# Kernel tuning notes

Measured on AMD Instinct MI355X. Metric: run time of the kernel, lower is better.

Reference implementation:

```python
import jax, jax.numpy as jnp
import numpy as np

N = 10000   # num nodes
E = 160000  # num edges (avg degree 16)
B = 8       # batch dim carried on node state
D = 64      # hidden_size


def setup_inputs() -> dict:
    key = jax.random.key(0)
    k1, k2, k3, k4, k5, k6 = jax.random.split(key, 6)
    state = jax.random.normal(k1, (N, B, D), jnp.float32)
    feature = jax.random.normal(k2, (N, 32), jnp.float32)  # unused by GAT math, kept for call signature
    weight = jax.random.normal(k3, (2 * D, D), jnp.float32) * 0.05
    src = jax.random.randint(k4, (E,), 0, N, jnp.int32)
    dst = jax.random.randint(k5, (E,), 0, N, jnp.int32)
    dist = jax.random.uniform(k6, (E, 1), jnp.float32)
    return dict(state=state, feature=feature, weight=weight, src=src, dst=dst, dist=dist)


def reference(state, feature, weight, src, dst, dist):
    # --- msg_edge: gather src/dst node states per edge ---
    src_state = state[src]                 # [E,B,D]
    dst_state = state[dst]                 # [E,B,D]
    es = jnp.concatenate([src_state, dst_state], axis=-1)          # [E,B,2D]
    alpha = jax.nn.leaky_relu(jnp.einsum('ebk,kd->ebd', es, weight),
                              negative_slope=0.2)                  # tf.nn.leaky_relu alpha=0.2
    alpha = alpha * dist[:, :, None]       # dist [E,1] broadcast to [E,1,1]

    # --- msg_reduce: segment softmax over incoming edges of each dst node ---
    amax = jax.ops.segment_max(alpha, dst, num_segments=N)         # [N,B,D]
    ex = jnp.exp(alpha - amax[dst])                                # stable exp
    denom = jax.ops.segment_sum(ex, dst, num_segments=N)           # [N,B,D]
    attn = ex / denom[dst]                                         # [E,B,D]

    # weighted sum of src states scattered back to dst nodes, then relu
    new_state = jax.nn.relu(jax.ops.segment_sum(attn * src_state, dst, num_segments=N))
    return new_state
```

## Files before the change

kernel.cpp:

```cpp
#include <hip/hip_runtime.h>
#include <hip/hip_fp16.h>
#include <math.h>

#define N_NODES 10000
#define N_EDGES 160000
#define B_ 8
#define D_ 64
#define BD 512
#define CAP 48
#define CAPR 56

typedef _Float16 f16x8 __attribute__((ext_vector_type(8)));
typedef float f32x4 __attribute__((ext_vector_type(4)));
typedef float f4v __attribute__((ext_vector_type(4)));
typedef unsigned int u32;

union HU { _Float16 f; unsigned short u; };
union HC { u32 u; __half2 h; };

__global__ void __launch_bounds__(256, 4) prep_kernel(
    const int* __restrict__ src, const int* __restrict__ dst,
    const float* __restrict__ dist, int* __restrict__ counts, u32* __restrict__ bucket,
    const float* __restrict__ state, const float* __restrict__ weight,
    u32* __restrict__ G, __half* __restrict__ Pd) {
    __shared__ _Float16 At[64 * 72];
    __shared__ char smemB[128 * 72 * 2];
    _Float16* Bt = (_Float16*)smemB;
    unsigned short* Ps2 = (unsigned short*)smemB;
    unsigned short* Ps  = (unsigned short*)(smemB + 8704);
    int bid = blockIdx.x;
    int tid = threadIdx.x;

    int s_e, d_e; float di_e;
    bool do_edge = tid < 128;
    if (do_edge) {
        int e = bid * 128 + tid;
        s_e = src[e];
        d_e = dst[e];
        di_e = dist[e];
    }

    int row0 = bid * 64;
    int wave = tid >> 6, lane = tid & 63;
    int quad = lane >> 4, m16 = lane & 15;
    int m_loc = wave * 16 + m16;

    const f4v* st4 = (const f4v*)(state + (size_t)row0 * 64);
    for (int i = tid; i < 1024; i += 256) {
        int r = i >> 4, c4 = (i & 15) << 2;
        f4v v = __builtin_nontemporal_load(&st4[i]);
        union { short4 s; _Float16 h[4]; } u;
        u.h[0] = (_Float16)v[0]; u.h[1] = (_Float16)v[1];
        u.h[2] = (_Float16)v[2]; u.h[3] = (_Float16)v[3];
        *(short4*)&At[r * 72 + c4] = u.s;
    }
    const f4v* w4 = (const f4v*)weight;
    for (int i = tid; i < 2048; i += 256) {
        int r = i >> 4, c4 = (i & 15) << 2;
        f4v v = w4[i];
        int h = r >> 6, k = r & 63;
        int nb = h * 64 + c4;
        Bt[(nb + 0) * 72 + k] = (_Float16)v[0];
        Bt[(nb + 1) * 72 + k] = (_Float16)v[1];
        Bt[(nb + 2) * 72 + k] = (_Float16)v[2];
        Bt[(nb + 3) * 72 + k] = (_Float16)v[3];
    }

    if (do_edge) {
        int pos = atomicAdd(&counts[d_e], 1);
        if (pos < CAP) {
            unsigned short hd = __half_as_ushort(__float2half_rn(di_e * 1.44269504f));
            bucket[d_e * CAPR + pos] = (u32)s_e | ((u32)hd << 16);
        }
    }
    __syncthreads();

    f16x8 bf0[8], bf1[8];
#pragma unroll
    for (int tcol = 0; tcol < 8; tcol++) {
        int n = tcol * 16 + m16;
        bf0[tcol] = *(const f16x8*)&Bt[n * 72 + quad * 8];
        bf1[tcol] = *(const f16x8*)&Bt[n * 72 + 32 + quad * 8];
    }
    f16x8 a0 = *(const f16x8*)&At[m_loc * 72 + quad * 8];
    f16x8 a1 = *(const f16x8*)&At[m_loc * 72 + 32 + quad * 8];
    __syncthreads();

#pragma unroll
    for (int tcol = 0; tcol < 8; tcol++) {
        int n = tcol * 16 + m16;
        f32x4 acc = {0.f, 0.f, 0.f, 0.f};
        acc = __builtin_amdgcn_mfma_f32_16x16x32_f16(a0, bf0[tcol], acc, 0, 0, 0);
        acc = __builtin_amdgcn_mfma_f32_16x16x32_f16(a1, bf1[tcol], acc, 0, 0, 0);
#pragma unroll
        for (int r = 0; r < 4; r++) {
            int ml = wave * 16 + quad * 4 + r;
            unsigned short ph = __half_as_ushort(__float2half_rn(acc[r]));
            if (tcol < 4) Ps2[ml * 68 + n] = ph;
            else          Ps[ml * 64 + (n - 64)] = ph;
        }
    }
    __syncthreads();

    const u32* Ps2w = (const u32*)Ps2;
    const u32* Atw = (const u32*)At;
    for (int i = tid; i < 1024; i += 256) {
        int row = i >> 4, q = i & 15;
        int m = row0 + row;
        size_t base = (size_t)(m >> 3) * 512 + (size_t)(m & 7) * 64;
        u32 p01 = Ps2w[row * 34 + q * 2];
        u32 p23 = Ps2w[row * 34 + q * 2 + 1];
        u32 x01 = Atw[row * 36 + q * 2];
        u32 x23 = Atw[row * 36 + q * 2 + 1];
        float4 v = make_float4(__uint_as_float(p01), __uint_as_float(p23),
                               __uint_as_float(x01), __uint_as_float(x23));
        *(float4*)&G[base + q * 4] = v;
    }
    for (int i = tid; i < 512; i += 256) {
        int row = i >> 3, seg = i & 7;
        int m = row0 + row;
        size_t base = (size_t)(m >> 3) * 512 + (size_t)(m & 7) * 64;
        *(float4*)&Pd[base + seg * 8] = *(const float4*)&Ps[row * 64 + seg * 8];
    }
}

__global__ void __launch_bounds__(256) gat_aggregate(
    const u32* __restrict__ G,
    const __half* __restrict__ Pds,
    const int* __restrict__ counts,
    const u32* __restrict__ bucket,
    float* __restrict__ out) {
    int wave = threadIdx.x >> 6;
    int lane = threadIdx.x & 63;
    int n = (blockIdx.x << 2) + wave;

    int offA = lane * 4;
    int offB = offA + 256;

    int cnt = counts[n]; if (cnt > CAP) cnt = CAP;
    const u32* ep = bucket + n * CAPR;

    union { double d; __half2 h[2]; } pdA, pdB;
    pdA.d = *(const double*)(Pds + (size_t)n * 512 + offA);
    pdB.d = *(const double*)(Pds + (size_t)n * 512 + offB);

    const __half2 c06 = __float2half2_rn(0.6f);
    const __half2 c04 = __float2half2_rn(0.4f);
    __half2 zero = __float2half2_rn(0.f);
    __half2 lA0 = zero, lA1 = zero, oA0 = zero, oA1 = zero;
    __half2 lB0 = zero, lB1 = zero, oB0 = zero, oB1 = zero;

    auto lrexp = [&](__half2 z, __half2 dd) -> __half2 {
        HC zz, az; zz.h = z;
        az.u = zz.u & 0x7fff7fffu;
        __half2 lk = __hfma2(az.h, c04, __hmul2(z, c06));
        __half2 aa = __hmul2(lk, dd);
        return __halves2half2(hexp2(__low2half(aa)), hexp2(__high2half(aa)));
    };

    auto body = [&](float4 g1, float4 g2, __half2 dd) {
        union { float4 f; __half2 h[4]; } u1, u2; u1.f = g1; u2.f = g2;
        __half2 e;
        e = lrexp(__hadd2(u1.h[0], pdA.h[0]), dd); lA0 = __hadd2(lA0, e); oA0 = __hfma2(e, u1.h[2], oA0);
        e = lrexp(__hadd2(u1.h[1], pdA.h[1]), dd); lA1 = __hadd2(lA1, e); oA1 = __hfma2(e, u1.h[3], oA1);
        e = lrexp(__hadd2(u2.h[0], pdB.h[0]), dd); lB0 = __hadd2(lB0, e); oB0 = __hfma2(e, u2.h[2], oB0);
        e = lrexp(__hadd2(u2.h[1], pdB.h[1]), dd); lB1 = __hadd2(lB1, e); oB1 = __hfma2(e, u2.h[3], oB1);
    };

    for (int j = 0; j < cnt; j += 2) {
        u32 ra = ep[j];
        bool two = (j + 1) < cnt;
        u32 rb = two ? ep[j + 1] : 0u;
        const u32* pa = G + (size_t)(ra & 0xffffu) * 512;
        float4 ga1 = *(const float4*)(pa + offA);
        float4 ga2 = *(const float4*)(pa + offB);
        float4 gb1, gb2;
        if (two) {
            const u32* pb = G + (size_t)(rb & 0xffffu) * 512;
            gb1 = *(const float4*)(pb + offA);
            gb2 = *(const float4*)(pb + offB);
        }
        __half ha = __ushort_as_half((unsigned short)(ra >> 16));
        body(ga1, ga2, __halves2half2(ha, ha));
        if (two) {
            __half hb = __ushort_as_half((unsigned short)(rb >> 16));
            body(gb1, gb2, __halves2half2(hb, hb));
        }
    }

    float* op = out + (size_t)n * BD;
    float4 rA, rB;
    if (cnt > 0) {
        rA.x = fmaxf(__low2float(oA0)  * __builtin_amdgcn_rcpf(__low2float(lA0)),  0.f);
        rA.y = fmaxf(__high2float(oA0) * __builtin_amdgcn_rcpf(__high2float(lA0)), 0.f);
        rA.z = fmaxf(__low2float(oA1)  * __builtin_amdgcn_rcpf(__low2float(lA1)),  0.f);
        rA.w = fmaxf(__high2float(oA1) * __builtin_amdgcn_rcpf(__high2float(lA1)), 0.f);
        rB.x = fmaxf(__low2float(oB0)  * __builtin_amdgcn_rcpf(__low2float(lB0)),  0.f);
        rB.y = fmaxf(__high2float(oB0) * __builtin_amdgcn_rcpf(__high2float(lB0)), 0.f);
        rB.z = fmaxf(__low2float(oB1)  * __builtin_amdgcn_rcpf(__low2float(lB1)),  0.f);
        rB.w = fmaxf(__high2float(oB1) * __builtin_amdgcn_rcpf(__high2float(lB1)), 0.f);
    } else {
        rA = make_float4(0.f, 0.f, 0.f, 0.f);
        rB = rA;
    }
    *(float4*)(op + offA) = rA;
    *(float4*)(op + offB) = rB;
}

extern "C" void kernel_launch(void* const* d_in, const int* in_sizes, int n_in,
                              void* d_out, int out_size, void* d_ws, size_t ws_size,
                              hipStream_t stream) {
    const float* state  = (const float*)d_in[0];
    const float* weight = (const float*)d_in[2];
    const int*   src    = (const int*)d_in[3];
    const int*   dst    = (const int*)d_in[4];
    const float* dist   = (const float*)d_in[5];

    u32*    G      = (u32*)d_ws;
    __half* Pd     = (__half*)(G + (size_t)N_NODES * 512);
    u32*    bucket = (u32*)(Pd + (size_t)N_NODES * 512);
    int*    counts = (int*)(bucket + (size_t)N_NODES * CAPR);

    hipMemsetAsync(bucket, 0, ((size_t)N_NODES * CAPR + N_NODES) * sizeof(u32), stream);
    prep_kernel<<<1250, 256, 0, stream>>>(src, dst, dist, counts, bucket,
                                          state, weight, G, Pd);
    gat_aggregate<<<2500, 256, 0, stream>>>(G, Pd, counts, bucket, (float*)d_out);
}
```

Measured before the change: 146.2 us.

## Split gather table into four batch-pair planes and process two edges per wave

The gathered node table G and the Pd buffer are reorganised into four planes, each holding two of the eight batch slices per node. Each aggregate block now handles one plane, and the two halves of a wave process alternate edges, combined at the end with a cross-lane shuffle. The intent is a smaller per-plane working set that fits better in cache during random gathers, and more blocks for parallelism. The cost is four times as many blocks, repeated bucket and count reads per plane, and an odd-count padding trick that reads node 0's row and subtracts its contribution.

```diff
diff --git a/kernel.cpp b/kernel.cpp
--- a/kernel.cpp
+++ b/kernel.cpp
@@ -107,7 +107,9 @@
     for (int i = tid; i < 1024; i += 256) {
         int row = i >> 4, q = i & 15;
         int m = row0 + row;
-        size_t base = (size_t)(m >> 3) * 512 + (size_t)(m & 7) * 64;
+        int b = m & 7;
+        size_t base = (size_t)(b >> 1) * (N_NODES * 128)
+                    + (size_t)(m >> 3) * 128 + (size_t)(b & 1) * 64;
         u32 p01 = Ps2w[row * 34 + q * 2];
         u32 p23 = Ps2w[row * 34 + q * 2 + 1];
         u32 x01 = Atw[row * 36 + q * 2];
@@ -119,7 +121,9 @@
     for (int i = tid; i < 512; i += 256) {
         int row = i >> 3, seg = i & 7;
         int m = row0 + row;
-        size_t base = (size_t)(m >> 3) * 512 + (size_t)(m & 7) * 64;
+        int b = m & 7;
+        size_t base = (size_t)(b >> 1) * (N_NODES * 128)
+                    + (size_t)(m >> 3) * 128 + (size_t)(b & 1) * 64;
         *(float4*)&Pd[base + seg * 8] = *(const float4*)&Ps[row * 64 + seg * 8];
     }
 }
@@ -130,25 +134,28 @@
     const int* __restrict__ counts,
     const u32* __restrict__ bucket,
     float* __restrict__ out) {
+    int bid = blockIdx.x;
+    int bp = bid & 3;
+    int ng = bid >> 2;
     int wave = threadIdx.x >> 6;
     int lane = threadIdx.x & 63;
-    int n = (blockIdx.x << 2) + wave;
-
-    int offA = lane * 4;
-    int offB = offA + 256;
+    int n = ng * 4 + wave;
+    int e = lane >> 5;
+    int off = (lane & 31) * 4;
+
+    const u32* Gbp = G + (size_t)bp * (N_NODES * 128);
+    const __half* Pbp = Pds + (size_t)bp * (N_NODES * 128);
 
     int cnt = counts[n]; if (cnt > CAP) cnt = CAP;
     const u32* ep = bucket + n * CAPR;
 
-    union { double d; __half2 h[2]; } pdA, pdB;
-    pdA.d = *(const double*)(Pds + (size_t)n * 512 + offA);
-    pdB.d = *(const double*)(Pds + (size_t)n * 512 + offB);
+    union { double d; __half2 h[2]; } pd;
+    pd.d = *(const double*)(Pbp + n * 128 + off);
 
     const __half2 c06 = __float2half2_rn(0.6f);
     const __half2 c04 = __float2half2_rn(0.4f);
     __half2 zero = __float2half2_rn(0.f);
-    __half2 lA0 = zero, lA1 = zero, oA0 = zero, oA1 = zero;
-    __half2 lB0 = zero, lB1 = zero, oB0 = zero, oB1 = zero;
+    __half2 l01 = zero, l23 = zero, o01 = zero, o23 = zero;
 
     auto lrexp = [&](__half2 z, __half2 dd) -> __half2 {
         HC zz, az; zz.h = z;
@@ -158,53 +165,54 @@
         return __halves2half2(hexp2(__low2half(aa)), hexp2(__high2half(aa)));
     };
 
-    auto body = [&](float4 g1, float4 g2, __half2 dd) {
-        union { float4 f; __half2 h[4]; } u1, u2; u1.f = g1; u2.f = g2;
-        __half2 e;
-        e = lrexp(__hadd2(u1.h[0], pdA.h[0]), dd); lA0 = __hadd2(lA0, e); oA0 = __hfma2(e, u1.h[2], oA0);
-        e = lrexp(__hadd2(u1.h[1], pdA.h[1]), dd); lA1 = __hadd2(lA1, e); oA1 = __hfma2(e, u1.h[3], oA1);
-        e = lrexp(__hadd2(u2.h[0], pdB.h[0]), dd); lB0 = __hadd2(lB0, e); oB0 = __hfma2(e, u2.h[2], oB0);
-        e = lrexp(__hadd2(u2.h[1], pdB.h[1]), dd); lB1 = __hadd2(lB1, e); oB1 = __hfma2(e, u2.h[3], oB1);
-    };
-
-    for (int j = 0; j < cnt; j += 2) {
-        u32 ra = ep[j];
-        bool two = (j + 1) < cnt;
-        u32 rb = two ? ep[j + 1] : 0u;
-        const u32* pa = G + (size_t)(ra & 0xffffu) * 512;
-        float4 ga1 = *(const float4*)(pa + offA);
-        float4 ga2 = *(const float4*)(pa + offB);
-        float4 gb1, gb2;
-        if (two) {
-            const u32* pb = G + (size_t)(rb & 0xffffu) * 512;
-            gb1 = *(const float4*)(pb + offA);
-            gb2 = *(const float4*)(pb + offB);
-        }
-        __half ha = __ushort_as_half((unsigned short)(ra >> 16));
-        body(ga1, ga2, __halves2half2(ha, ha));
-        if (two) {
-            __half hb = __ushort_as_half((unsigned short)(rb >> 16));
-            body(gb1, gb2, __halves2half2(hb, hb));
-        }
-    }
-
-    float* op = out + (size_t)n * BD;
-    float4 rA, rB;
-    if (cnt > 0) {
-        rA.x = fmaxf(__low2float(oA0)  * __builtin_amdgcn_rcpf(__low2float(lA0)),  0.f);
-        rA.y = fmaxf(__high2float(oA0) * __builtin_amdgcn_rcpf(__high2float(lA0)), 0.f);
-        rA.z = fmaxf(__low2float(oA1)  * __builtin_amdgcn_rcpf(__low2float(lA1)),  0.f);
-        rA.w = fmaxf(__high2float(oA1) * __builtin_amdgcn_rcpf(__high2float(lA1)), 0.f);
-        rB.x = fmaxf(__low2float(oB0)  * __builtin_amdgcn_rcpf(__low2float(lB0)),  0.f);
-        rB.y = fmaxf(__high2float(oB0) * __builtin_amdgcn_rcpf(__high2float(lB0)), 0.f);
-        rB.z = fmaxf(__low2float(oB1)  * __builtin_amdgcn_rcpf(__low2float(lB1)),  0.f);
-        rB.w = fmaxf(__high2float(oB1) * __builtin_amdgcn_rcpf(__high2float(lB1)), 0.f);
-    } else {
-        rA = make_float4(0.f, 0.f, 0.f, 0.f);
-        rB = rA;
-    }
-    *(float4*)(op + offA) = rA;
-    *(float4*)(op + offB) = rB;
+    int padded = (cnt + 1) & ~1;
+    if (padded > 0) {
+        u32 r = ep[e];
+        for (int j = 0; j < padded; j += 2) {
+            u32 rn = ep[j + 2 + e];
+            const u32* p = Gbp + (size_t)(r & 0xffffu) * 128 + off;
+            float4 g = *(const float4*)p;
+            __half hd = __ushort_as_half((unsigned short)(r >> 16));
+            __half2 dd = __halves2half2(hd, hd);
+            union { float4 f; __half2 h[4]; } u; u.f = g;
+            __half2 ex;
+            ex = lrexp(__hadd2(u.h[0], pd.h[0]), dd);
+            l01 = __hadd2(l01, ex); o01 = __hfma2(ex, u.h[2], o01);
+            ex = lrexp(__hadd2(u.h[1], pd.h[1]), dd);
+            l23 = __hadd2(l23, ex); o23 = __hfma2(ex, u.h[3], o23);
+            r = rn;
+        }
+        if (cnt & 1) {
+            float4 g0 = *(const float4*)(Gbp + off);
+            union { float4 f; __half2 h[4]; } u0; u0.f = g0;
+            if (e) {
+                __half2 one = __float2half2_rn(1.f);
+                l01 = __hsub2(l01, one);
+                l23 = __hsub2(l23, one);
+                o01 = __hsub2(o01, u0.h[2]);
+                o23 = __hsub2(o23, u0.h[3]);
+            }
+        }
+    }
+
+    HC c;
+    c.u = (u32)__shfl_xor((int)((HC){.h = l01}).u, 32, 64); l01 = __hadd2(l01, c.h);
+    c.u = (u32)__shfl_xor((int)((HC){.h = l23}).u, 32, 64); l23 = __hadd2(l23, c.h);
+    c.u = (u32)__shfl_xor((int)((HC){.h = o01}).u, 32, 64); o01 = __hadd2(o01, c.h);
+    c.u = (u32)__shfl_xor((int)((HC){.h = o23}).u, 32, 64); o23 = __hadd2(o23, c.h);
+
+    if (e == 0) {
+        float4 r;
+        if (cnt > 0) {
+            r.x = fmaxf(__low2float(o01)  * __builtin_amdgcn_rcpf(__low2float(l01)),  0.f);
+            r.y = fmaxf(__high2float(o01) * __builtin_amdgcn_rcpf(__high2float(l01)), 0.f);
+            r.z = fmaxf(__low2float(o23)  * __builtin_amdgcn_rcpf(__low2float(l23)),  0.f);
+            r.w = fmaxf(__high2float(o23) * __builtin_amdgcn_rcpf(__high2float(l23)), 0.f);
+        } else {
+            r = make_float4(0.f, 0.f, 0.f, 0.f);
+        }
+        *(float4*)(out + (size_t)n * BD + bp * 128 + off) = r;
+    }
 }
 
 extern "C" void kernel_launch(void* const* d_in, const int* in_sizes, int n_in,
@@ -217,12 +225,12 @@
     const float* dist   = (const float*)d_in[5];
 
     u32*    G      = (u32*)d_ws;
-    __half* Pd     = (__half*)(G + (size_t)N_NODES * 512);
-    u32*    bucket = (u32*)(Pd + (size_t)N_NODES * 512);
+    __half* Pd     = (__half*)(G + (size_t)4 * N_NODES * 128);
+    u32*    bucket = (u32*)(Pd + (size_t)4 * N_NODES * 128);
     int*    counts = (int*)(bucket + (size_t)N_NODES * CAPR);
 
     hipMemsetAsync(bucket, 0, ((size_t)N_NODES * CAPR + N_NODES) * sizeof(u32), stream);
     prep_kernel<<<1250, 256, 0, stream>>>(src, dst, dist, counts, bucket,
                                           state, weight, G, Pd);
-    gat_aggregate<<<2500, 256, 0, stream>>>(G, Pd, counts, bucket, (float*)d_out);
+    gat_aggregate<<<10000, 256, 0, stream>>>(G, Pd, counts, bucket, (float*)d_out);
 }
```

Measured after the change: 141.8 us. -3.1%, faster.
